# Optimization experiments

Measured on AMD Instinct MI355X. Metric: run time of the kernel, lower is better.

The kernel has to match this reference:

```python
import jax, jax.numpy as jnp
import numpy as np

NUM_CLASSES = 64  # matches labels fill_max
EMB_SCALE = 0.1   # keeps pairwise distances small so exp() stays finite (same regime as trained embeddings)


def setup_inputs() -> dict:
    key = jax.random.key(0)
    k1, k2 = jax.random.split(key)
    embeddings = jax.random.normal(k1, (8192, 128), dtype=jnp.float32) * EMB_SCALE
    labels = jax.random.randint(k2, (8192,), 0, NUM_CLASSES, dtype=jnp.int64 if jax.config.jax_enable_x64 else jnp.int32)
    return {"embeddings": embeddings, "labels": labels}


def reference(embeddings, labels):
    # Squared-euclidean distance matrix: ||xi||^2 + ||xj||^2 - 2 xi.xj   [N,N]
    sq = jnp.sum(embeddings * embeddings, axis=1)
    D = sq[:, None] + sq[None, :] - 2.0 * (embeddings @ embeddings.T)

    N = embeddings.shape[0]
    same = labels[:, None] == labels[None, :]          # [N,N] same-label mask
    neg = jnp.logical_not(same)

    # Z_i = sum over negatives n of exp(D[i,n]); then for pair (i,j):
    # sum_n exp(D[i,n] - D[i,j]) = Z_i * exp(-D[i,j])  (exact same math, factored)
    Z = jnp.sum(jnp.where(neg, jnp.exp(D), 0.0), axis=1)  # [N]

    # anchor-positive pairs: combinations(label_indices, 2) => i<j, same label
    iu = jnp.arange(N)
    pair_mask = same & (iu[:, None] < iu[None, :])

    # per-pair loss: log(1 + sum_n exp(D[a,n] - D[a,p]))
    L = jnp.log1p(Z[:, None] * jnp.exp(-D))            # [N,N]

    row_sum = jnp.sum(jnp.where(pair_mask, L, 0.0), axis=1)   # anchor i contributes pairs with label labels[i]
    row_cnt = jnp.sum(pair_mask, axis=1).astype(L.dtype)

    label_sum = jax.ops.segment_sum(row_sum, labels, num_segments=NUM_CLASSES)
    label_cnt = jax.ops.segment_sum(row_cnt, labels, num_segments=NUM_CLASSES)

    valid = label_cnt > 0                               # classes with >=2 members
    label_mean = jnp.where(valid, label_sum / jnp.maximum(label_cnt, 1.0), 0.0)
    n_valid = jnp.sum(valid)
    loss = jnp.sum(label_mean) / jnp.maximum(n_valid, 1).astype(L.dtype)
    return loss
```

## Files before the change

kernel.cpp:

```cpp
#include <hip/hip_runtime.h>
#include <hip/hip_bf16.h>
#include <math.h>

#define KD 128
#define NCLS 64
#define LOG2E 1.4426950408889634f
#define NEG2L -2.8853900817779268f
#define POS2L 2.8853900817779268f

typedef __attribute__((ext_vector_type(8))) short short8;
typedef __attribute__((ext_vector_type(4))) float f32x4;

__device__ inline void gload_lds16(const void* g, void* l) {
    __builtin_amdgcn_global_load_lds((const __attribute__((address_space(1))) unsigned int*)g,
                                     (__attribute__((address_space(3))) unsigned int*)l,
                                     16, 0, 0);
}
__device__ __forceinline__ float vexp2(float x) { float r; asm("v_exp_f32 %0, %1" : "=v"(r) : "v"(x)); return r; }
__device__ __forceinline__ float vlog2(float x) { float r; asm("v_log_f32 %0, %1" : "=v"(r) : "v"(x)); return r; }

__global__ __launch_bounds__(256) void cvtprep_kernel(const float* __restrict__ emb,
                                                      short* __restrict__ embb,
                                                      float* __restrict__ s2, int N) {
    int w = (blockIdx.x * 256 + threadIdx.x) >> 6;
    int l = threadIdx.x & 63;
    int r0 = w * 4;
    if (r0 >= N) return;
    float2 v[4];
#pragma unroll
    for (int r = 0; r < 4; ++r)
        v[r] = *(const float2*)&emb[(size_t)(r0 + r) * KD + l * 2];
    float s[4];
#pragma unroll
    for (int r = 0; r < 4; ++r) {
        s[r] = v[r].x * v[r].x + v[r].y * v[r].y;
        __hip_bfloat16 h0 = __float2bfloat16(v[r].x);
        __hip_bfloat16 h1 = __float2bfloat16(v[r].y);
        unsigned int pk = ((unsigned int)*(unsigned short*)&h1 << 16) | (unsigned int)*(unsigned short*)&h0;
        *(unsigned int*)&embb[(size_t)(r0 + r) * KD + l * 2] = pk;
    }
#pragma unroll
    for (int r = 0; r < 4; ++r)
        for (int m = 32; m; m >>= 1) s[r] += __shfl_xor(s[r], m, 64);
    if (l == 0) {
#pragma unroll
        for (int r = 0; r < 4; ++r) s2[r0 + r] = s[r] * LOG2E;
    }
}

__global__ __launch_bounds__(1024) void scan_scatter_kernel(const int* __restrict__ lab,
                                                            int* __restrict__ cnt,
                                                            int* __restrict__ off,
                                                            int* __restrict__ list, int N) {
    __shared__ int cntL[NCLS], offL[NCLS], curL[NCLS];
    int tid = threadIdx.x;
    if (tid < NCLS) cntL[tid] = 0;
    __syncthreads();
    for (int i = tid; i < N; i += 1024) atomicAdd(&cntL[lab[i]], 1);
    __syncthreads();
    if (tid < NCLS) {
        int v = cntL[tid];
        int s = v;
        for (int m = 1; m < 64; m <<= 1) {
            int t = __shfl_up(s, m, 64);
            if (tid >= m) s += t;
        }
        offL[tid] = s - v;
        curL[tid] = 0;
        off[tid] = s - v;
        cnt[tid] = v;
    }
    __syncthreads();
    for (int i = tid; i < N; i += 1024) {
        int c = lab[i];
        int p = atomicAdd(&curL[c], 1);
        list[offL[c] + p] = i;
    }
}

__global__ __launch_bounds__(256, 2) void zmain_kernel(const short* __restrict__ embb,
                                                       const float* __restrict__ s2,
                                                       float* __restrict__ Z, int N) {
    __shared__ short8 As8[128 * 16];
    __shared__ short8 Bs8[128 * 16];

    const int tid = threadIdx.x;
    const int w = tid >> 6, l = tid & 63;
    const int wr = w >> 1, wc = w & 1;
    const int g = blockIdx.x, it = blockIdx.y;
    const int i0 = it * 128;
    const short8* embv = (const short8*)embb;

    int dlist[5];
    int nd = 4;
#pragma unroll
    for (int t = 0; t < 4; ++t) dlist[t] = g * 4 + t;
    if (g == 7 && it < 32) dlist[nd++] = 32;

#pragma unroll
    for (int itr = 0; itr < 8; ++itr) {
        int lr = w * 32 + itr * 4 + (l >> 4);
        int c = (l & 15) ^ (lr & 7);
        gload_lds16(embv + (size_t)(i0 + lr) * 16 + c, &As8[w * 512 + itr * 64]);
    }
    {
        int j0 = ((it + dlist[0]) & 63) * 128;
#pragma unroll
        for (int itr = 0; itr < 8; ++itr) {
            int lr = w * 32 + itr * 4 + (l >> 4);
            int c = (l & 15) ^ (lr & 7);
            gload_lds16(embv + (size_t)(j0 + lr) * 16 + c, &Bs8[w * 512 + itr * 64]);
        }
    }

    float s2i[4][4];
#pragma unroll
    for (int mi = 0; mi < 4; ++mi)
#pragma unroll
        for (int r = 0; r < 4; ++r)
            s2i[mi][r] = s2[i0 + wr * 64 + mi * 16 + (l >> 4) * 4 + r];
    float zsum[4][4];
#pragma unroll
    for (int mi = 0; mi < 4; ++mi)
#pragma unroll
        for (int r = 0; r < 4; ++r) zsum[mi][r] = 0.f;

    __syncthreads();

    short8 af[4][4];
#pragma unroll
    for (int mi = 0; mi < 4; ++mi) {
        int row = wr * 64 + mi * 16 + (l & 15);
        int rs = row * 16, rx = row & 7;
#pragma unroll
        for (int ks = 0; ks < 4; ++ks) {
            int kc = ks * 4 + (l >> 4);
            af[mi][ks] = As8[rs + (kc ^ rx)];
        }
    }
    __syncthreads();

    for (int t = 0; t < nd; ++t) {
        const int d = dlist[t];
        const int j0 = ((it + d) & 63) * 128;
        short8* rb = (t & 1) ? As8 : Bs8;
        short8* sb = (t & 1) ? Bs8 : As8;
        if (t + 1 < nd) {
            int j1 = ((it + dlist[t + 1]) & 63) * 128;
#pragma unroll
            for (int itr = 0; itr < 8; ++itr) {
                int lr = w * 32 + itr * 4 + (l >> 4);
                int c = (l & 15) ^ (lr & 7);
                gload_lds16(embv + (size_t)(j1 + lr) * 16 + c, &sb[w * 512 + itr * 64]);
            }
        }

        f32x4 acc[4][4];
#pragma unroll
        for (int mi = 0; mi < 4; ++mi)
#pragma unroll
            for (int ni = 0; ni < 4; ++ni) acc[mi][ni] = (f32x4){0.f, 0.f, 0.f, 0.f};

#pragma unroll
        for (int ks = 0; ks < 4; ++ks) {
            short8 bf[4];
            int kc = ks * 4 + (l >> 4);
#pragma unroll
            for (int ni = 0; ni < 4; ++ni) {
                int row = wc * 64 + ni * 16 + (l & 15);
                bf[ni] = rb[row * 16 + (kc ^ (row & 7))];
            }
#pragma unroll
            for (int mi = 0; mi < 4; ++mi)
#pragma unroll
                for (int ni = 0; ni < 4; ++ni)
                    acc[mi][ni] = __builtin_amdgcn_mfma_f32_16x16x32_bf16(af[mi][ks], bf[ni], acc[mi][ni], 0, 0, 0);
        }

        float s2j[4];
#pragma unroll
        for (int ni = 0; ni < 4; ++ni)
            s2j[ni] = s2[j0 + wc * 64 + ni * 16 + (l & 15)];
        float cs[4] = {0.f, 0.f, 0.f, 0.f};
#pragma unroll
        for (int mi = 0; mi < 4; ++mi)
#pragma unroll
            for (int ni = 0; ni < 4; ++ni)
#pragma unroll
                for (int r = 0; r < 4; ++r) {
                    float e = vexp2(fmaf(NEG2L, acc[mi][ni][r], s2i[mi][r] + s2j[ni]));
                    zsum[mi][r] += e;
                    cs[ni] += e;
                }
        if (d > 0) {
#pragma unroll
            for (int ni = 0; ni < 4; ++ni) {
                float v = cs[ni];
                v += __shfl_xor(v, 16, 64);
                v += __shfl_xor(v, 32, 64);
                if ((l >> 4) == 0)
                    atomicAdd(&Z[j0 + wc * 64 + ni * 16 + (l & 15)], v);
            }
        }
        __syncthreads();
    }

#pragma unroll
    for (int mi = 0; mi < 4; ++mi)
#pragma unroll
        for (int r = 0; r < 4; ++r) {
            float v = zsum[mi][r];
            v += __shfl_xor(v, 1, 64);
            v += __shfl_xor(v, 2, 64);
            v += __shfl_xor(v, 4, 64);
            v += __shfl_xor(v, 8, 64);
            if ((l & 15) == 0)
                atomicAdd(&Z[i0 + wr * 64 + mi * 16 + (l >> 4) * 4 + r], v);
        }
}

__device__ __forceinline__ void gram_quad(const short8* Ms8, int l, int wr, int wc,
                                          int qi, int qj, f32x4 acc[4][4]) {
#pragma unroll
    for (int mi = 0; mi < 4; ++mi)
#pragma unroll
        for (int ni = 0; ni < 4; ++ni) acc[mi][ni] = (f32x4){0.f, 0.f, 0.f, 0.f};
#pragma unroll
    for (int ks = 0; ks < 4; ++ks) {
        short8 af[4], bf[4];
        int kc = ks * 4 + (l >> 4);
#pragma unroll
        for (int mi = 0; mi < 4; ++mi) {
            int row = qi * 128 + wr * 64 + mi * 16 + (l & 15);
            af[mi] = Ms8[row * 16 + (kc ^ (row & 7))];
        }
#pragma unroll
        for (int ni = 0; ni < 4; ++ni) {
            int row = qj * 128 + wc * 64 + ni * 16 + (l & 15);
            bf[ni] = Ms8[row * 16 + (kc ^ (row & 7))];
        }
#pragma unroll
        for (int mi = 0; mi < 4; ++mi)
#pragma unroll
            for (int ni = 0; ni < 4; ++ni)
                acc[mi][ni] = __builtin_amdgcn_mfma_f32_16x16x32_bf16(af[mi], bf[ni], acc[mi][ni], 0, 0, 0);
    }
}

__global__ __launch_bounds__(256, 2) void loss_kernel(const short* __restrict__ embb,
                                                      const float* __restrict__ s2,
                                                      const float* __restrict__ Z,
                                                      const int* __restrict__ cnt,
                                                      const int* __restrict__ off,
                                                      const int* __restrict__ list,
                                                      float* __restrict__ lsum) {
    __shared__ short8 Ms8[256 * 16];
    __shared__ float s2L[256], zfL[256], zsubL[256];
    __shared__ int gidL[256];
    __shared__ float red[4];

    const int h = blockIdx.x, c = blockIdx.y;
    const int k = cnt[c], base = off[c];
    if (k < 2) return;
    const int kp = min(k, 256);
    if (h == 1 && kp <= 128) return;

    const int tid = threadIdx.x;
    const int w = tid >> 6, l = tid & 63;
    const int wr = w >> 1, wc = w & 1;
    const short8* embv = (const short8*)embb;

    {
        int pos = tid;
        int gg = list[base + min(pos, k - 1)];
        bool ok = pos < k;
        s2L[pos] = ok ? s2[gg] : 0.f;
        gidL[pos] = ok ? gg : 0x7fffffff;
        zsubL[pos] = 0.f;
    }
#pragma unroll
    for (int itr = 0; itr < 16; ++itr) {
        int grp = w * 16 + itr;
        if (grp * 4 >= kp) break;
        int lr = grp * 4 + (l >> 4);
        int ch = (l & 15) ^ (lr & 7);
        int gg = list[base + min(lr, k - 1)];
        gload_lds16(embv + (size_t)gg * 16 + ch, &Ms8[grp * 64]);
    }
    __syncthreads();

    const int two = (kp > 128);
    f32x4 acc[4][4];

    for (int qq = 0; qq <= 2 * two; ++qq) {
        int qi = (qq == 2) ? 1 : 0;
        int qj = (qq == 0) ? 0 : 1;
        gram_quad(Ms8, l, wr, wc, qi, qj, acc);
        float rowsum[4][4];
#pragma unroll
        for (int mi = 0; mi < 4; ++mi)
#pragma unroll
            for (int r = 0; r < 4; ++r) rowsum[mi][r] = 0.f;
        float colsum[4] = {0.f, 0.f, 0.f, 0.f};
#pragma unroll
        for (int mi = 0; mi < 4; ++mi)
#pragma unroll
            for (int ni = 0; ni < 4; ++ni) {
                int pB = qi * 128 + wr * 64 + mi * 16 + (l >> 4) * 4;
                int qL = qj * 128 + wc * 64 + ni * 16 + (l & 15);
                float sj = s2L[qL];
#pragma unroll
                for (int r = 0; r < 4; ++r) {
                    float e = vexp2(fmaf(NEG2L, acc[mi][ni][r], s2L[pB + r] + sj));
                    e = ((pB + r) < k && qL < k) ? e : 0.f;
                    rowsum[mi][r] += e;
                    colsum[ni] += e;
                }
            }
#pragma unroll
        for (int mi = 0; mi < 4; ++mi)
#pragma unroll
            for (int r = 0; r < 4; ++r) {
                float v = rowsum[mi][r];
                v += __shfl_xor(v, 1, 64);
                v += __shfl_xor(v, 2, 64);
                v += __shfl_xor(v, 4, 64);
                v += __shfl_xor(v, 8, 64);
                if ((l & 15) == 0)
                    atomicAdd(&zsubL[qi * 128 + wr * 64 + mi * 16 + (l >> 4) * 4 + r], v);
            }
        if (qi != qj) {
#pragma unroll
            for (int ni = 0; ni < 4; ++ni) {
                float v = colsum[ni];
                v += __shfl_xor(v, 16, 64);
                v += __shfl_xor(v, 32, 64);
                if ((l >> 4) == 0)
                    atomicAdd(&zsubL[qj * 128 + wc * 64 + ni * 16 + (l & 15)], v);
            }
        }
    }
    __syncthreads();
    {
        int pos = tid;
        zfL[pos] = (pos < k) ? (Z[gidL[pos]] - zsubL[pos]) : 0.f;
    }
    __syncthreads();

    float part = 0.f;
    int q0 = (h == 0) ? 0 : 2;
    int q1 = (h == 0) ? (two ? 1 : 0) : 2;
    for (int qq = q0; qq <= q1; ++qq) {
        int qi = (qq == 2) ? 1 : 0;
        int qj = (qq == 0) ? 0 : 1;
        gram_quad(Ms8, l, wr, wc, qi, qj, acc);
#pragma unroll
        for (int mi = 0; mi < 4; ++mi)
#pragma unroll
            for (int ni = 0; ni < 4; ++ni) {
                int qL = qj * 128 + wc * 64 + ni * 16 + (l & 15);
                float sj = s2L[qL];
                float zq = zfL[qL];
                int gb = gidL[qL];
#pragma unroll
                for (int r = 0; r < 4; ++r) {
                    int pL = qi * 128 + wr * 64 + mi * 16 + (l >> 4) * 4 + r;
                    bool valid = (pL < qL) && (qL < k);
                    float arg = fmaf(POS2L, acc[mi][ni][r], -(s2L[pL] + sj));
                    arg = valid ? arg : -160.f;
                    float e = vexp2(arg);
                    float z = (gidL[pL] < gb) ? zfL[pL] : zq;
                    part += vlog2(fmaf(z, e, 1.0f));
                }
            }
    }

    for (int m = 32; m; m >>= 1) part += __shfl_xor(part, m, 64);
    if (l == 0) red[w] = part;
    __syncthreads();
    if (tid == 0)
        atomicAdd(&lsum[c], red[0] + red[1] + red[2] + red[3]);
}

__global__ void fin_kernel(const float* __restrict__ lsum, const int* __restrict__ cnt,
                           float* __restrict__ out) {
    int c = threadIdx.x;
    float mean = 0.f;
    int valid = 0;
    if (c < NCLS) {
        long k = cnt[c];
        long np = k * (k - 1) / 2;
        if (np > 0) { mean = lsum[c] * 0.6931471805599453f / (float)np; valid = 1; }
    }
    float sm = mean;
    int sv = valid;
    for (int m = 32; m; m >>= 1) {
        sm += __shfl_xor(sm, m, 64);
        sv += __shfl_xor(sv, m, 64);
    }
    if (c == 0) out[0] = sm / (float)max(sv, 1);
}

extern "C" void kernel_launch(void* const* d_in, const int* in_sizes, int n_in,
                              void* d_out, int out_size, void* d_ws, size_t ws_size,
                              hipStream_t stream) {
    const float* emb = (const float*)d_in[0];
    const int* lab = (const int*)d_in[1];
    float* out = (float*)d_out;
    const int N = in_sizes[1];

    float* ws = (float*)d_ws;
    float* Z = ws;
    float* lsum = ws + N;
    int* cnt = (int*)(ws + N + NCLS);
    int* off = cnt + NCLS;
    int* list = off + NCLS;
    float* s2 = (float*)(list + N);
    short* embb = (short*)(s2 + N);

    hipMemsetAsync(Z, 0, (size_t)(N + NCLS) * 4, stream);
    scan_scatter_kernel<<<1, 1024, 0, stream>>>(lab, cnt, off, list, N);
    cvtprep_kernel<<<N / 16, 256, 0, stream>>>(emb, embb, s2, N);
    dim3 zgrid(8, N / 128);
    zmain_kernel<<<zgrid, 256, 0, stream>>>(embb, s2, Z, N);
    dim3 lgrid(2, NCLS);
    loss_kernel<<<lgrid, 256, 0, stream>>>(embb, s2, Z, cnt, off, list, lsum);
    fin_kernel<<<1, 64, 0, stream>>>(lsum, cnt, out);
}
```

Measured before the change: 113.3 us.

## Fuse prep kernels and memset, fold final reduction into loss kernel

Merges the label scan/scatter, bf16 conversion and norm computation into one prep kernel, with the last block doing the scan while the others convert rows and zero Z. The memset is removed because prep_kernel now zeroes Z, lsum and a completion counter. The separate finalisation kernel is replaced by a last-block-done pattern in loss_kernel that uses an atomic counter and a threadfence. The intent is to cut launch overhead and serialization across five launches, at the cost of a single-block scan sitting on the critical path of prep and extra fences in the loss kernel.

```diff
diff --git a/kernel.cpp b/kernel.cpp
--- a/kernel.cpp
+++ b/kernel.cpp
@@ -7,6 +7,7 @@
 #define LOG2E 1.4426950408889634f
 #define NEG2L -2.8853900817779268f
 #define POS2L 2.8853900817779268f
+#define LN2 0.6931471805599453f
 
 typedef __attribute__((ext_vector_type(8))) short short8;
 typedef __attribute__((ext_vector_type(4))) float f32x4;
@@ -19,62 +20,68 @@
 __device__ __forceinline__ float vexp2(float x) { float r; asm("v_exp_f32 %0, %1" : "=v"(r) : "v"(x)); return r; }
 __device__ __forceinline__ float vlog2(float x) { float r; asm("v_log_f32 %0, %1" : "=v"(r) : "v"(x)); return r; }
 
-__global__ __launch_bounds__(256) void cvtprep_kernel(const float* __restrict__ emb,
-                                                      short* __restrict__ embb,
-                                                      float* __restrict__ s2, int N) {
-    int w = (blockIdx.x * 256 + threadIdx.x) >> 6;
-    int l = threadIdx.x & 63;
-    int r0 = w * 4;
-    if (r0 >= N) return;
-    float2 v[4];
-#pragma unroll
-    for (int r = 0; r < 4; ++r)
-        v[r] = *(const float2*)&emb[(size_t)(r0 + r) * KD + l * 2];
-    float s[4];
-#pragma unroll
-    for (int r = 0; r < 4; ++r) {
-        s[r] = v[r].x * v[r].x + v[r].y * v[r].y;
-        __hip_bfloat16 h0 = __float2bfloat16(v[r].x);
-        __hip_bfloat16 h1 = __float2bfloat16(v[r].y);
-        unsigned int pk = ((unsigned int)*(unsigned short*)&h1 << 16) | (unsigned int)*(unsigned short*)&h0;
-        *(unsigned int*)&embb[(size_t)(r0 + r) * KD + l * 2] = pk;
-    }
-#pragma unroll
-    for (int r = 0; r < 4; ++r)
-        for (int m = 32; m; m >>= 1) s[r] += __shfl_xor(s[r], m, 64);
-    if (l == 0) {
-#pragma unroll
-        for (int r = 0; r < 4; ++r) s2[r0 + r] = s[r] * LOG2E;
-    }
-}
-
-__global__ __launch_bounds__(1024) void scan_scatter_kernel(const int* __restrict__ lab,
-                                                            int* __restrict__ cnt,
-                                                            int* __restrict__ off,
-                                                            int* __restrict__ list, int N) {
-    __shared__ int cntL[NCLS], offL[NCLS], curL[NCLS];
-    int tid = threadIdx.x;
-    if (tid < NCLS) cntL[tid] = 0;
-    __syncthreads();
-    for (int i = tid; i < N; i += 1024) atomicAdd(&cntL[lab[i]], 1);
-    __syncthreads();
-    if (tid < NCLS) {
-        int v = cntL[tid];
-        int s = v;
-        for (int m = 1; m < 64; m <<= 1) {
-            int t = __shfl_up(s, m, 64);
-            if (tid >= m) s += t;
-        }
-        offL[tid] = s - v;
-        curL[tid] = 0;
-        off[tid] = s - v;
-        cnt[tid] = v;
-    }
-    __syncthreads();
-    for (int i = tid; i < N; i += 1024) {
-        int c = lab[i];
-        int p = atomicAdd(&curL[c], 1);
-        list[offL[c] + p] = i;
+__global__ __launch_bounds__(256) void prep_kernel(const float* __restrict__ emb,
+                                                   const int* __restrict__ lab,
+                                                   short* __restrict__ embb,
+                                                   float* __restrict__ s2,
+                                                   float* __restrict__ Z,
+                                                   float* __restrict__ lsum,
+                                                   int* __restrict__ cnt,
+                                                   int* __restrict__ off,
+                                                   int* __restrict__ list,
+                                                   int* __restrict__ ctr, int N) {
+    const int tid = threadIdx.x;
+    if (blockIdx.x == gridDim.x - 1) {
+        __shared__ int cntL[NCLS], offL[NCLS], curL[NCLS];
+        if (tid < NCLS) cntL[tid] = 0;
+        __syncthreads();
+        for (int i = tid; i < N; i += 256) atomicAdd(&cntL[lab[i]], 1);
+        __syncthreads();
+        if (tid < NCLS) {
+            int v = cntL[tid];
+            int s = v;
+            for (int m = 1; m < 64; m <<= 1) {
+                int t2 = __shfl_up(s, m, 64);
+                if (tid >= m) s += t2;
+            }
+            offL[tid] = s - v;
+            curL[tid] = 0;
+            off[tid] = s - v;
+            cnt[tid] = v;
+            lsum[tid] = 0.f;
+        }
+        if (tid == 0) ctr[0] = 0;
+        __syncthreads();
+        for (int i = tid; i < N; i += 256) {
+            int c = lab[i];
+            int p = atomicAdd(&curL[c], 1);
+            list[offL[c] + p] = i;
+        }
+    } else {
+        const int b = blockIdx.x;
+        const int r0 = b * 16;
+        const size_t base = (size_t)r0 * KD;
+        float4 a = *(const float4*)&emb[base + (size_t)tid * 8];
+        float4 bb = *(const float4*)&emb[base + (size_t)tid * 8 + 4];
+        short8 o;
+        __hip_bfloat16 h;
+        h = __float2bfloat16(a.x);  o[0] = *(short*)&h;
+        h = __float2bfloat16(a.y);  o[1] = *(short*)&h;
+        h = __float2bfloat16(a.z);  o[2] = *(short*)&h;
+        h = __float2bfloat16(a.w);  o[3] = *(short*)&h;
+        h = __float2bfloat16(bb.x); o[4] = *(short*)&h;
+        h = __float2bfloat16(bb.y); o[5] = *(short*)&h;
+        h = __float2bfloat16(bb.z); o[6] = *(short*)&h;
+        h = __float2bfloat16(bb.w); o[7] = *(short*)&h;
+        *(short8*)&embb[base + (size_t)tid * 8] = o;
+        float s = a.x * a.x + a.y * a.y + a.z * a.z + a.w * a.w
+                + bb.x * bb.x + bb.y * bb.y + bb.z * bb.z + bb.w * bb.w;
+        s += __shfl_xor(s, 1, 64);
+        s += __shfl_xor(s, 2, 64);
+        s += __shfl_xor(s, 4, 64);
+        s += __shfl_xor(s, 8, 64);
+        if ((tid & 15) == 0) s2[r0 + (tid >> 4)] = s * LOG2E;
+        if (tid < 16) Z[r0 + tid] = 0.f;
     }
 }
 
@@ -90,12 +97,7 @@
     const int g = blockIdx.x, it = blockIdx.y;
     const int i0 = it * 128;
     const short8* embv = (const short8*)embb;
-
-    int dlist[5];
-    int nd = 4;
-#pragma unroll
-    for (int t = 0; t < 4; ++t) dlist[t] = g * 4 + t;
-    if (g == 7 && it < 32) dlist[nd++] = 32;
+    const int nd = 4 + ((g == 7 && it < 32) ? 1 : 0);
 
 #pragma unroll
     for (int itr = 0; itr < 8; ++itr) {
@@ -104,7 +106,7 @@
         gload_lds16(embv + (size_t)(i0 + lr) * 16 + c, &As8[w * 512 + itr * 64]);
     }
     {
-        int j0 = ((it + dlist[0]) & 63) * 128;
+        int j0 = ((it + g * 4) & 63) * 128;
 #pragma unroll
         for (int itr = 0; itr < 8; ++itr) {
             int lr = w * 32 + itr * 4 + (l >> 4);
@@ -141,12 +143,13 @@
     __syncthreads();
 
     for (int t = 0; t < nd; ++t) {
-        const int d = dlist[t];
+        const int d = (t < 4) ? (g * 4 + t) : 32;
         const int j0 = ((it + d) & 63) * 128;
         short8* rb = (t & 1) ? As8 : Bs8;
         short8* sb = (t & 1) ? Bs8 : As8;
         if (t + 1 < nd) {
-            int j1 = ((it + dlist[t + 1]) & 63) * 128;
+            const int d1 = (t + 1 < 4) ? (g * 4 + t + 1) : 32;
+            int j1 = ((it + d1) & 63) * 128;
 #pragma unroll
             for (int itr = 0; itr < 8; ++itr) {
                 int lr = w * 32 + itr * 4 + (l >> 4);
@@ -253,152 +256,153 @@
                                                       const int* __restrict__ cnt,
                                                       const int* __restrict__ off,
                                                       const int* __restrict__ list,
-                                                      float* __restrict__ lsum) {
+                                                      float* __restrict__ lsum,
+                                                      int* __restrict__ ctr,
+                                                      float* __restrict__ out) {
     __shared__ short8 Ms8[256 * 16];
     __shared__ float s2L[256], zfL[256], zsubL[256];
     __shared__ int gidL[256];
     __shared__ float red[4];
+    __shared__ int lastB;
 
     const int h = blockIdx.x, c = blockIdx.y;
     const int k = cnt[c], base = off[c];
-    if (k < 2) return;
     const int kp = min(k, 256);
-    if (h == 1 && kp <= 128) return;
-
     const int tid = threadIdx.x;
     const int w = tid >> 6, l = tid & 63;
     const int wr = w >> 1, wc = w & 1;
     const short8* embv = (const short8*)embb;
 
-    {
-        int pos = tid;
-        int gg = list[base + min(pos, k - 1)];
-        bool ok = pos < k;
-        s2L[pos] = ok ? s2[gg] : 0.f;
-        gidL[pos] = ok ? gg : 0x7fffffff;
-        zsubL[pos] = 0.f;
-    }
-#pragma unroll
-    for (int itr = 0; itr < 16; ++itr) {
-        int grp = w * 16 + itr;
-        if (grp * 4 >= kp) break;
-        int lr = grp * 4 + (l >> 4);
-        int ch = (l & 15) ^ (lr & 7);
-        int gg = list[base + min(lr, k - 1)];
-        gload_lds16(embv + (size_t)gg * 16 + ch, &Ms8[grp * 64]);
-    }
+    const bool active = (k >= 2) && !(h == 1 && kp <= 128);
+    if (active) {
+        {
+            int gg = list[base + min(tid, k - 1)];
+            bool ok = tid < k;
+            s2L[tid] = ok ? s2[gg] : 0.f;
+            gidL[tid] = ok ? gg : 0x7fffffff;
+            zsubL[tid] = 0.f;
+        }
+#pragma unroll
+        for (int itr = 0; itr < 16; ++itr) {
+            int grp = w * 16 + itr;
+            if (grp * 4 >= kp) break;
+            int lr = grp * 4 + (l >> 4);
+            int ch = (l & 15) ^ (lr & 7);
+            int gg = list[base + min(lr, k - 1)];
+            gload_lds16(embv + (size_t)gg * 16 + ch, &Ms8[grp * 64]);
+        }
+        __syncthreads();
+
+        const int two = (kp > 128);
+        f32x4 acc[4][4];
+
+        for (int qq = 0; qq <= 2 * two; ++qq) {
+            int qi = (qq == 2) ? 1 : 0;
+            int qj = (qq == 0) ? 0 : 1;
+            gram_quad(Ms8, l, wr, wc, qi, qj, acc);
+            float rowsum[4][4];
+#pragma unroll
+            for (int mi = 0; mi < 4; ++mi)
+#pragma unroll
+                for (int r = 0; r < 4; ++r) rowsum[mi][r] = 0.f;
+            float colsum[4] = {0.f, 0.f, 0.f, 0.f};
+#pragma unroll
+            for (int mi = 0; mi < 4; ++mi)
+#pragma unroll
+                for (int ni = 0; ni < 4; ++ni) {
+                    int pB = qi * 128 + wr * 64 + mi * 16 + (l >> 4) * 4;
+                    int qL = qj * 128 + wc * 64 + ni * 16 + (l & 15);
+                    float sj = s2L[qL];
+#pragma unroll
+                    for (int r = 0; r < 4; ++r) {
+                        float e = vexp2(fmaf(NEG2L, acc[mi][ni][r], s2L[pB + r] + sj));
+                        e = ((pB + r) < k && qL < k) ? e : 0.f;
+                        rowsum[mi][r] += e;
+                        colsum[ni] += e;
+                    }
+                }
+#pragma unroll
+            for (int mi = 0; mi < 4; ++mi)
+#pragma unroll
+                for (int r = 0; r < 4; ++r) {
+                    float v = rowsum[mi][r];
+                    v += __shfl_xor(v, 1, 64);
+                    v += __shfl_xor(v, 2, 64);
+                    v += __shfl_xor(v, 4, 64);
+                    v += __shfl_xor(v, 8, 64);
+                    if ((l & 15) == 0)
+                        atomicAdd(&zsubL[qi * 128 + wr * 64 + mi * 16 + (l >> 4) * 4 + r], v);
+                }
+            if (qi != qj) {
+#pragma unroll
+                for (int ni = 0; ni < 4; ++ni) {
+                    float v = colsum[ni];
+                    v += __shfl_xor(v, 16, 64);
+                    v += __shfl_xor(v, 32, 64);
+                    if ((l >> 4) == 0)
+                        atomicAdd(&zsubL[qj * 128 + wc * 64 + ni * 16 + (l & 15)], v);
+                }
+            }
+        }
+        __syncthreads();
+        zfL[tid] = (tid < k) ? (Z[gidL[tid]] - zsubL[tid]) : 0.f;
+        __syncthreads();
+
+        float part = 0.f;
+        int q0 = (h == 0) ? 0 : 2;
+        int q1 = (h == 0) ? (two ? 1 : 0) : 2;
+        for (int qq = q0; qq <= q1; ++qq) {
+            int qi = (qq == 2) ? 1 : 0;
+            int qj = (qq == 0) ? 0 : 1;
+            gram_quad(Ms8, l, wr, wc, qi, qj, acc);
+#pragma unroll
+            for (int mi = 0; mi < 4; ++mi)
+#pragma unroll
+                for (int ni = 0; ni < 4; ++ni) {
+                    int qL = qj * 128 + wc * 64 + ni * 16 + (l & 15);
+                    float sj = s2L[qL];
+                    float zq = zfL[qL];
+                    int gb = gidL[qL];
+#pragma unroll
+                    for (int r = 0; r < 4; ++r) {
+                        int pL = qi * 128 + wr * 64 + mi * 16 + (l >> 4) * 4 + r;
+                        bool valid = (pL < qL) && (qL < k);
+                        float arg = fmaf(POS2L, acc[mi][ni][r], -(s2L[pL] + sj));
+                        arg = valid ? arg : -160.f;
+                        float e = vexp2(arg);
+                        float z = (gidL[pL] < gb) ? zfL[pL] : zq;
+                        part += vlog2(fmaf(z, e, 1.0f));
+                    }
+                }
+        }
+
+        for (int m = 32; m; m >>= 1) part += __shfl_xor(part, m, 64);
+        if (l == 0) red[w] = part;
+        __syncthreads();
+        if (tid == 0)
+            atomicAdd(&lsum[c], red[0] + red[1] + red[2] + red[3]);
+    }
+
+    __threadfence();
+    if (tid == 0) lastB = (atomicAdd(ctr, 1) == 2 * NCLS - 1);
     __syncthreads();
-
-    const int two = (kp > 128);
-    f32x4 acc[4][4];
-
-    for (int qq = 0; qq <= 2 * two; ++qq) {
-        int qi = (qq == 2) ? 1 : 0;
-        int qj = (qq == 0) ? 0 : 1;
-        gram_quad(Ms8, l, wr, wc, qi, qj, acc);
-        float rowsum[4][4];
-#pragma unroll
-        for (int mi = 0; mi < 4; ++mi)
-#pragma unroll
-            for (int r = 0; r < 4; ++r) rowsum[mi][r] = 0.f;
-        float colsum[4] = {0.f, 0.f, 0.f, 0.f};
-#pragma unroll
-        for (int mi = 0; mi < 4; ++mi)
-#pragma unroll
-            for (int ni = 0; ni < 4; ++ni) {
-                int pB = qi * 128 + wr * 64 + mi * 16 + (l >> 4) * 4;
-                int qL = qj * 128 + wc * 64 + ni * 16 + (l & 15);
-                float sj = s2L[qL];
-#pragma unroll
-                for (int r = 0; r < 4; ++r) {
-                    float e = vexp2(fmaf(NEG2L, acc[mi][ni][r], s2L[pB + r] + sj));
-                    e = ((pB + r) < k && qL < k) ? e : 0.f;
-                    rowsum[mi][r] += e;
-                    colsum[ni] += e;
-                }
-            }
-#pragma unroll
-        for (int mi = 0; mi < 4; ++mi)
-#pragma unroll
-            for (int r = 0; r < 4; ++r) {
-                float v = rowsum[mi][r];
-                v += __shfl_xor(v, 1, 64);
-                v += __shfl_xor(v, 2, 64);
-                v += __shfl_xor(v, 4, 64);
-                v += __shfl_xor(v, 8, 64);
-                if ((l & 15) == 0)
-                    atomicAdd(&zsubL[qi * 128 + wr * 64 + mi * 16 + (l >> 4) * 4 + r], v);
-            }
-        if (qi != qj) {
-#pragma unroll
-            for (int ni = 0; ni < 4; ++ni) {
-                float v = colsum[ni];
-                v += __shfl_xor(v, 16, 64);
-                v += __shfl_xor(v, 32, 64);
-                if ((l >> 4) == 0)
-                    atomicAdd(&zsubL[qj * 128 + wc * 64 + ni * 16 + (l & 15)], v);
-            }
-        }
-    }
-    __syncthreads();
-    {
-        int pos = tid;
-        zfL[pos] = (pos < k) ? (Z[gidL[pos]] - zsubL[pos]) : 0.f;
-    }
-    __syncthreads();
-
-    float part = 0.f;
-    int q0 = (h == 0) ? 0 : 2;
-    int q1 = (h == 0) ? (two ? 1 : 0) : 2;
-    for (int qq = q0; qq <= q1; ++qq) {
-        int qi = (qq == 2) ? 1 : 0;
-        int qj = (qq == 0) ? 0 : 1;
-        gram_quad(Ms8, l, wr, wc, qi, qj, acc);
-#pragma unroll
-        for (int mi = 0; mi < 4; ++mi)
-#pragma unroll
-            for (int ni = 0; ni < 4; ++ni) {
-                int qL = qj * 128 + wc * 64 + ni * 16 + (l & 15);
-                float sj = s2L[qL];
-                float zq = zfL[qL];
-                int gb = gidL[qL];
-#pragma unroll
-                for (int r = 0; r < 4; ++r) {
-                    int pL = qi * 128 + wr * 64 + mi * 16 + (l >> 4) * 4 + r;
-                    bool valid = (pL < qL) && (qL < k);
-                    float arg = fmaf(POS2L, acc[mi][ni][r], -(s2L[pL] + sj));
-                    arg = valid ? arg : -160.f;
-                    float e = vexp2(arg);
-                    float z = (gidL[pL] < gb) ? zfL[pL] : zq;
-                    part += vlog2(fmaf(z, e, 1.0f));
-                }
-            }
-    }
-
-    for (int m = 32; m; m >>= 1) part += __shfl_xor(part, m, 64);
-    if (l == 0) red[w] = part;
-    __syncthreads();
-    if (tid == 0)
-        atomicAdd(&lsum[c], red[0] + red[1] + red[2] + red[3]);
-}
-
-__global__ void fin_kernel(const float* __restrict__ lsum, const int* __restrict__ cnt,
-                           float* __restrict__ out) {
-    int c = threadIdx.x;
-    float mean = 0.f;
-    int valid = 0;
-    if (c < NCLS) {
-        long k = cnt[c];
-        long np = k * (k - 1) / 2;
-        if (np > 0) { mean = lsum[c] * 0.6931471805599453f / (float)np; valid = 1; }
-    }
-    float sm = mean;
-    int sv = valid;
-    for (int m = 32; m; m >>= 1) {
-        sm += __shfl_xor(sm, m, 64);
-        sv += __shfl_xor(sv, m, 64);
-    }
-    if (c == 0) out[0] = sm / (float)max(sv, 1);
+    if (lastB) {
+        __threadfence();
+        if (tid < 64) {
+            int cc = tid;
+            float ls = atomicAdd(&lsum[cc], 0.0f);
+            int kk = atomicAdd((int*)&cnt[cc], 0);
+            float mean = 0.f;
+            int valid = 0;
+            long np = (long)kk * (kk - 1) / 2;
+            if (np > 0) { mean = ls * LN2 / (float)np; valid = 1; }
+            for (int m = 32; m; m >>= 1) {
+                mean += __shfl_xor(mean, m, 64);
+                valid += __shfl_xor(valid, m, 64);
+            }
+            if (cc == 0) out[0] = mean / (float)max(valid, 1);
+        }
+    }
 }
 
 extern "C" void kernel_launch(void* const* d_in, const int* in_sizes, int n_in,
@@ -414,16 +418,14 @@
     float* lsum = ws + N;
     int* cnt = (int*)(ws + N + NCLS);
     int* off = cnt + NCLS;
-    int* list = off + NCLS;
+    int* ctr = off + NCLS;
+    int* list = ctr + NCLS;
     float* s2 = (float*)(list + N);
     short* embb = (short*)(s2 + N);
 
-    hipMemsetAsync(Z, 0, (size_t)(N + NCLS) * 4, stream);
-    scan_scatter_kernel<<<1, 1024, 0, stream>>>(lab, cnt, off, list, N);
-    cvtprep_kernel<<<N / 16, 256, 0, stream>>>(emb, embb, s2, N);
+    prep_kernel<<<N / 16 + 1, 256, 0, stream>>>(emb, lab, embb, s2, Z, lsum, cnt, off, list, ctr, N);
     dim3 zgrid(8, N / 128);
     zmain_kernel<<<zgrid, 256, 0, stream>>>(embb, s2, Z, N);
     dim3 lgrid(2, NCLS);
-    loss_kernel<<<lgrid, 256, 0, stream>>>(embb, s2, Z, cnt, off, list, lsum);
-    fin_kernel<<<1, 64, 0, stream>>>(lsum, cnt, out);
-}
+    loss_kernel<<<lgrid, 256, 0, stream>>>(embb, s2, Z, cnt, off, list, lsum, ctr, out);
+}
```

Result: slower. 122.5 us (+8.1%).
